# Kernel optimization log

Hardware: AMD Instinct MI355X
Metric: run time of the kernel (lower is better)

## Reference

```python
import jax, jax.numpy as jnp
import numpy as np

B, N, F, FP, H = 4, 2048, 64, 32, 4
BN_EPS = 1e-3  # tf.layers.batch_normalization default


def setup_inputs() -> dict:
    key = jax.random.key(0)
    ks = jax.random.split(key, 8)
    x = jax.random.normal(ks[0], (B, N, F), dtype=jnp.float32)
    adj = jax.random.uniform(ks[1], (B, N, N), dtype=jnp.float32)
    attn_mask = jnp.zeros((B, N, N), dtype=jnp.float32)
    # per-head parameters stacked on leading head axis
    W = jax.random.normal(ks[2], (H, F, FP), dtype=jnp.float32) * 0.1
    a_self = jax.random.normal(ks[3], (H, FP), dtype=jnp.float32) * 0.1
    a_neigh = jax.random.normal(ks[4], (H, FP), dtype=jnp.float32) * 0.1
    bias = jnp.zeros((H, FP), dtype=jnp.float32)
    # batch-norm (inference) params over concat dim H*FP
    gamma = jnp.ones((H * FP,), dtype=jnp.float32)
    beta = jnp.zeros((H * FP,), dtype=jnp.float32)
    mov_mean = jnp.zeros((H * FP,), dtype=jnp.float32)
    mov_var = jnp.ones((H * FP,), dtype=jnp.float32)
    return dict(x=x, adj=adj, attn_mask=attn_mask, W=W, a_self=a_self,
                a_neigh=a_neigh, bias=bias, gamma=gamma, beta=beta,
                mov_mean=mov_mean, mov_var=mov_var)


def reference(x, adj, attn_mask, W, a_self, a_neigh, bias, gamma, beta,
              mov_mean, mov_var):
    # features per head: [B, H, N, FP]
    feats = jnp.einsum('bnf,hfd->bhnd', x, W)
    s = jnp.einsum('bhnd,hd->bhn', feats, a_self)    # attn_for_self
    t = jnp.einsum('bhnd,hd->bhn', feats, a_neigh)   # attn_for_neighs
    dense = s[..., :, None] + t[..., None, :]        # [B, H, N, N]
    dense = jnp.where(dense > 0, dense, 0.2 * dense)  # LeakyReLU(0.2)
    dense = dense + attn_mask[:, None]
    alpha = jax.nn.softmax(dense, axis=-1)
    alpha = alpha * adj[:, None]                     # include_ew=True
    # eval mode: dropout is identity
    node_feats = jnp.einsum('bhnm,bhmd->bhnd', alpha, feats) + bias[None, :, None, :]
    # attention stats losses
    nonz = (alpha != 0).sum(axis=-1)                 # [B, H, N]
    deg = (adj != 0).sum(axis=-1)                    # [B, N]
    uloss = jnp.sum(jnp.mean((nonz - deg[:, None, :]).astype(jnp.float32), axis=-1))
    eloss = jnp.sum(jnp.mean(jnp.sum(jnp.abs(alpha), axis=-1), axis=-1))
    # concat heads -> [B, N, H*FP]
    out = jnp.transpose(node_feats, (0, 2, 1, 3)).reshape(B, N, H * FP)
    # batch norm, inference mode
    out = (out - mov_mean) * jax.lax.rsqrt(mov_var + BN_EPS) * gamma + beta
    return jax.nn.relu(out), uloss, eloss
```

## Files before the change

kernel.cpp:

```cpp
#include <hip/hip_runtime.h>


#define B_ 4
#define N_ 2048
#define F_ 64
#define FP_ 32
#define H_ 4
#define C_ 128
#define IT_ 16
#define ITILES_ (N_ / IT_)
#define JCA_ 2
#define JSPANA_ (N_ / JCA_)
#define JST_ 128
#define APAD_ 132

typedef __attribute__((ext_vector_type(8))) short short8v;
typedef __attribute__((ext_vector_type(4))) float f32x4;

__device__ __forceinline__ unsigned short f2bf(float f) {
    unsigned u = __float_as_uint(f);
    u += 0x7fffu + ((u >> 16) & 1u);
    return (unsigned short)(u >> 16);
}

__global__ __launch_bounds__(256) void prep_kernel(
    const float* __restrict__ x, const float* __restrict__ W,
    const float* __restrict__ a_self, const float* __restrict__ a_neigh,
    unsigned short* __restrict__ featsT, float* __restrict__ sbuf,
    float* __restrict__ tbuf)
{
    int blk = blockIdx.x;
    int b = blk >> 5, nt = blk & 31;
    int n0 = nt << 6;
    int t = threadIdx.x, h = t >> 6, lane = t & 63;
    int quad = lane >> 4, col = lane & 15;

    short8v bw[2][2];
    const float* Wh = W + (size_t)h * F_ * FP_;
#pragma unroll
    for (int kc = 0; kc < 2; ++kc)
#pragma unroll
        for (int dt = 0; dt < 2; ++dt)
#pragma unroll
            for (int e = 0; e < 8; ++e) {
                int f = kc * 32 + quad * 8 + e;
                bw[kc][dt][e] = (short)f2bf(Wh[f * FP_ + dt * 16 + col]);
            }
    float as0 = a_self[h * FP_ + col],  as1 = a_self[h * FP_ + 16 + col];
    float an0 = a_neigh[h * FP_ + col], an1 = a_neigh[h * FP_ + 16 + col];
    size_t hrow = ((size_t)b * H_ + h) * N_;
    size_t ftb  = ((size_t)b * H_ + h) * FP_;

    for (int ms = 0; ms < 4; ++ms) {
        int row = n0 + ms * 16 + col;
        const float* xr = x + ((size_t)b * N_ + row) * F_;
        f32x4 acc0 = {0.f, 0.f, 0.f, 0.f}, acc1 = {0.f, 0.f, 0.f, 0.f};
#pragma unroll
        for (int kc = 0; kc < 2; ++kc) {
            float4 x0 = *(const float4*)(xr + kc * 32 + quad * 8);
            float4 x1 = *(const float4*)(xr + kc * 32 + quad * 8 + 4);
            short8v av;
            av[0] = (short)f2bf(x0.x); av[1] = (short)f2bf(x0.y);
            av[2] = (short)f2bf(x0.z); av[3] = (short)f2bf(x0.w);
            av[4] = (short)f2bf(x1.x); av[5] = (short)f2bf(x1.y);
            av[6] = (short)f2bf(x1.z); av[7] = (short)f2bf(x1.w);
            acc0 = __builtin_amdgcn_mfma_f32_16x16x32_bf16(av, bw[kc][0], acc0, 0, 0, 0);
            acc1 = __builtin_amdgcn_mfma_f32_16x16x32_bf16(av, bw[kc][1], acc1, 0, 0, 0);
        }
        {
            ushort4 v0, v1;
            v0.x = f2bf(acc0[0]); v0.y = f2bf(acc0[1]);
            v0.z = f2bf(acc0[2]); v0.w = f2bf(acc0[3]);
            v1.x = f2bf(acc1[0]); v1.y = f2bf(acc1[1]);
            v1.z = f2bf(acc1[2]); v1.w = f2bf(acc1[3]);
            size_t nidx = (size_t)n0 + ms * 16 + quad * 4;
            *(ushort4*)(featsT + (ftb + col) * N_ + nidx)      = v0;
            *(ushort4*)(featsT + (ftb + 16 + col) * N_ + nidx) = v1;
        }
#pragma unroll
        for (int rr = 0; rr < 4; ++rr) {
            float sv = acc0[rr] * as0 + acc1[rr] * as1;
            float tv = acc0[rr] * an0 + acc1[rr] * an1;
#pragma unroll
            for (int off = 8; off; off >>= 1) {
                sv += __shfl_down(sv, off);
                tv += __shfl_down(tv, off);
            }
            if (col == 0) {
                int n = n0 + ms * 16 + quad * 4 + rr;
                sbuf[hrow + n] = sv;
                tbuf[hrow + n] = tv;
            }
        }
    }
}

__global__ __launch_bounds__(256) void attn_kernel(
    const float* __restrict__ adj, const float* __restrict__ msk,
    const unsigned short* __restrict__ featsT,
    const float* __restrict__ sbuf, const float* __restrict__ tbuf,
    float* __restrict__ part, float* __restrict__ lpart)
{
    __shared__ float lds_adj[IT_ * APAD_];
    __shared__ float lds_msk[IT_ * APAD_];

    int blk = blockIdx.x;
    int jc = blk & (JCA_ - 1);
    int it = (blk >> 1) & (ITILES_ - 1);
    int b  = blk >> 8;
    int t = threadIdx.x, h = t >> 6, lane = t & 63;
    int quad = lane >> 4, r = lane & 15;
    int i0 = it * IT_;
    int jbase = jc * JSPANA_;

    size_t hrow = ((size_t)b * H_ + h) * N_;
    float si = sbuf[hrow + i0 + r];
    const float* trow = tbuf + hrow + jbase;
    const unsigned short* ft0 = featsT + (((size_t)b * H_ + h) * FP_ + r) * N_ + jbase;
    const unsigned short* ft1 = ft0 + (size_t)16 * N_;
    const float* adjb = adj + ((size_t)b * N_ + i0) * N_ + jbase;
    const float* mskb = msk + ((size_t)b * N_ + i0) * N_ + jbase;

    int srow = t >> 4, sj = (t & 15) * 8;

    f32x4 acc0 = {0.f, 0.f, 0.f, 0.f}, acc1 = {0.f, 0.f, 0.f, 0.f};
    float l = 0.f, A = 0.f, nz = 0.f;

    for (int st = 0; st < JSPANA_ / JST_; ++st) {
        int j0 = st * JST_;
        __syncthreads();
        {
            const float* ga = adjb + (size_t)srow * N_ + j0 + sj;
            const float* gm = mskb + (size_t)srow * N_ + j0 + sj;
            *(float4*)&lds_adj[srow * APAD_ + sj]     = *(const float4*)ga;
            *(float4*)&lds_adj[srow * APAD_ + sj + 4] = *(const float4*)(ga + 4);
            *(float4*)&lds_msk[srow * APAD_ + sj]     = *(const float4*)gm;
            *(float4*)&lds_msk[srow * APAD_ + sj + 4] = *(const float4*)(gm + 4);
        }
        __syncthreads();
#pragma unroll
        for (int kc = 0; kc < JST_ / 32; ++kc) {
            int jt = kc * 32 + quad * 8;
            int jl = j0 + jt;
            float4 a0 = *(const float4*)&lds_adj[r * APAD_ + jt];
            float4 a1 = *(const float4*)&lds_adj[r * APAD_ + jt + 4];
            float4 m0 = *(const float4*)&lds_msk[r * APAD_ + jt];
            float4 m1 = *(const float4*)&lds_msk[r * APAD_ + jt + 4];
            float4 t0 = *(const float4*)(trow + jl);
            float4 t1 = *(const float4*)(trow + jl + 4);
            short8v bv0 = *(const short8v*)(ft0 + jl);
            short8v bv1 = *(const short8v*)(ft1 + jl);
            float av[8] = {a0.x, a0.y, a0.z, a0.w, a1.x, a1.y, a1.z, a1.w};
            float mv[8] = {m0.x, m0.y, m0.z, m0.w, m1.x, m1.y, m1.z, m1.w};
            float tv[8] = {t0.x, t0.y, t0.z, t0.w, t1.x, t1.y, t1.z, t1.w};
            short8v ap;
#pragma unroll
            for (int q = 0; q < 8; ++q) {
                float dv = si + tv[q];
                dv = fmaxf(dv, 0.2f * dv);
                dv += mv[q];
                float e = __expf(dv);
                float p = e * av[q];
                l += e; A += p;
                nz += (av[q] == 0.f ? 1.f : 0.f) - (p == 0.f ? 1.f : 0.f);
                ap[q] = (short)f2bf(p);
            }
            acc0 = __builtin_amdgcn_mfma_f32_16x16x32_bf16(ap, bv0, acc0, 0, 0, 0);
            acc1 = __builtin_amdgcn_mfma_f32_16x16x32_bf16(ap, bv1, acc1, 0, 0, 0);
        }
    }
    l  += __shfl_down(l, 32);  l  += __shfl_down(l, 16);
    A  += __shfl_down(A, 32);  A  += __shfl_down(A, 16);
    nz += __shfl_down(nz, 32); nz += __shfl_down(nz, 16);

    size_t pb = ((((size_t)(b * H_ + h) * ITILES_ + it) * JCA_ + jc) * 2) * 256;
    *(f32x4*)&part[pb + lane * 4]       = acc0;
    *(f32x4*)&part[pb + 256 + lane * 4] = acc1;
    if (lane < 16) {
        size_t lb = (((size_t)(b * H_ + h) * ITILES_ + it) * JCA_ + jc) * 48;
        lpart[lb + lane]      = l;
        lpart[lb + 16 + lane] = A;
        lpart[lb + 32 + lane] = nz;
    }
}

__global__ __launch_bounds__(256) void final_kernel(
    const float* __restrict__ part, const float* __restrict__ lpart,
    const float* __restrict__ bias, const float* __restrict__ gamma,
    const float* __restrict__ beta, const float* __restrict__ mmean,
    const float* __restrict__ mvar, float2* __restrict__ lossbuf,
    float* __restrict__ out)
{
    __shared__ float ldsl[H_ * 16];
    __shared__ float ldso[IT_ * 132];
    int blk = blockIdx.x;
    int b = blk >> 7, it = blk & 127;
    int t = threadIdx.x, h = t >> 6, lane = t & 63;
    int quad = lane >> 4, col = lane & 15;

    size_t pb = (((size_t)(b * H_ + h) * ITILES_ + it) * JCA_) * 512;
    f32x4 C0 = *(const f32x4*)&part[pb + lane * 4];
    f32x4 C1 = *(const f32x4*)&part[pb + 256 + lane * 4];
    C0 += *(const f32x4*)&part[pb + 512 + lane * 4];
    C1 += *(const f32x4*)&part[pb + 768 + lane * 4];

    size_t lb = (((size_t)(b * H_ + h) * ITILES_ + it) * JCA_) * 48;
    if (lane < 16) {
        float lt  = lpart[lb + lane]      + lpart[lb + 48 + lane];
        float At  = lpart[lb + 16 + lane] + lpart[lb + 64 + lane];
        float nzt = lpart[lb + 32 + lane] + lpart[lb + 80 + lane];
        ldsl[h * 16 + lane] = lt;
        float u = nzt, e = At / lt;
#pragma unroll
        for (int off = 8; off; off >>= 1) { u += __shfl_down(u, off); e += __shfl_down(e, off); }
        if (lane == 0) lossbuf[blk * H_ + h] = make_float2(u, e);
    }
    __syncthreads();
#pragma unroll
    for (int dt = 0; dt < 2; ++dt) {
        int c = h * FP_ + dt * 16 + col;
        float sc = rsqrtf(mvar[c] + 1e-3f) * gamma[c];
        float sh = beta[c] - mmean[c] * sc;
        float bi = bias[c];
        f32x4 Cv = dt ? C1 : C0;
#pragma unroll
        for (int rr = 0; rr < 4; ++rr) {
            int row = quad * 4 + rr;
            float node = Cv[rr] / ldsl[h * 16 + row] + bi;
            float o = node * sc + sh;
            ldso[row * 132 + c] = o > 0.f ? o : 0.f;
        }
    }
    __syncthreads();
#pragma unroll
    for (int ps = 0; ps < 2; ++ps) {
        int row = ps * 8 + (t >> 5);
        int c4 = (t & 31) * 4;
        *(float4*)(out + ((size_t)b * N_ + it * IT_ + row) * C_ + c4) =
            *(const float4*)&ldso[row * 132 + c4];
    }
}

__global__ __launch_bounds__(256) void loss_kernel(
    const float2* __restrict__ lossbuf, float* __restrict__ out)
{
    float u = 0.f, e = 0.f;
    for (int idx = threadIdx.x; idx < B_ * ITILES_ * H_; idx += 256) {
        float2 v = lossbuf[idx];
        u += v.x; e += v.y;
    }
    __shared__ float su[256], se[256];
    su[threadIdx.x] = u; se[threadIdx.x] = e;
    __syncthreads();
    for (int o = 128; o; o >>= 1) {
        if (threadIdx.x < o) {
            su[threadIdx.x] += su[threadIdx.x + o];
            se[threadIdx.x] += se[threadIdx.x + o];
        }
        __syncthreads();
    }
    if (threadIdx.x == 0) {
        out[(size_t)B_ * N_ * C_]     = su[0] * (1.f / N_);
        out[(size_t)B_ * N_ * C_ + 1] = se[0] * (1.f / N_);
    }
}

extern "C" void kernel_launch(void* const* d_in, const int* in_sizes, int n_in,
                              void* d_out, int out_size, void* d_ws, size_t ws_size,
                              hipStream_t stream)
{
    const float* x         = (const float*)d_in[0];
    const float* adj       = (const float*)d_in[1];
    const float* attn_mask = (const float*)d_in[2];
    const float* W         = (const float*)d_in[3];
    const float* a_self    = (const float*)d_in[4];
    const float* a_neigh   = (const float*)d_in[5];
    const float* bias      = (const float*)d_in[6];
    const float* gamma     = (const float*)d_in[7];
    const float* beta      = (const float*)d_in[8];
    const float* mmean     = (const float*)d_in[9];
    const float* mvar      = (const float*)d_in[10];
    float* out = (float*)d_out;

    float* ws = (float*)d_ws;
    unsigned short* featsT = (unsigned short*)ws;
    float* sbuf  = ws + 524288;
    float* tbuf  = sbuf + (size_t)B_ * H_ * N_;
    float* part  = tbuf + (size_t)B_ * H_ * N_;
    float* lpart = part + (size_t)B_ * H_ * ITILES_ * JCA_ * 2 * 256;
    float* lossb = lpart + (size_t)B_ * H_ * ITILES_ * JCA_ * 48;

    hipLaunchKernelGGL(prep_kernel, dim3(B_ * 32), dim3(256), 0, stream,
                       x, W, a_self, a_neigh, featsT, sbuf, tbuf);
    hipLaunchKernelGGL(attn_kernel, dim3(B_ * ITILES_ * JCA_), dim3(256), 0, stream,
                       adj, attn_mask, featsT, sbuf, tbuf, part, lpart);
    hipLaunchKernelGGL(final_kernel, dim3(B_ * ITILES_), dim3(256), 0, stream,
                       part, lpart, bias, gamma, beta, mmean, mvar,
                       (float2*)lossb, out);
    hipLaunchKernelGGL(loss_kernel, dim3(1), dim3(256), 0, stream,
                       (const float2*)lossb, out);
}
```

Measured before the change: 209.6 us.

## Load adj/mask directly from global, drop LDS staging, split j into 4 chunks

The attention kernel no longer stages adj and mask tiles through shared memory with barriers. Each lane now reads its own row segment straight from global memory, which removes the __syncthreads and LDS round trip. The j-range is also split into 4 chunks instead of 2, doubling the grid for more parallelism, and the final kernel sums the extra partials in a loop. The risk is less coalesced global access, since each lane reads 32 bytes per row for 16 different rows, plus more partial-sum traffic. The launch grid must also match the new chunk count, which presumably happens in code not shown.

Measured after the change: 242.8 us. 1.16x slower.

```diff
diff --git a/kernel.cpp b/kernel.cpp
--- a/kernel.cpp
+++ b/kernel.cpp
@@ -9,10 +9,8 @@
 #define C_ 128
 #define IT_ 16
 #define ITILES_ (N_ / IT_)
-#define JCA_ 2
+#define JCA_ 4
 #define JSPANA_ (N_ / JCA_)
-#define JST_ 128
-#define APAD_ 132
 
 typedef __attribute__((ext_vector_type(8))) short short8v;
 typedef __attribute__((ext_vector_type(4))) float f32x4;
@@ -101,13 +99,10 @@
     const float* __restrict__ sbuf, const float* __restrict__ tbuf,
     float* __restrict__ part, float* __restrict__ lpart)
 {
-    __shared__ float lds_adj[IT_ * APAD_];
-    __shared__ float lds_msk[IT_ * APAD_];
-
     int blk = blockIdx.x;
     int jc = blk & (JCA_ - 1);
-    int it = (blk >> 1) & (ITILES_ - 1);
-    int b  = blk >> 8;
+    int it = (blk >> 2) & (ITILES_ - 1);
+    int b  = blk >> 9;
     int t = threadIdx.x, h = t >> 6, lane = t & 63;
     int quad = lane >> 4, r = lane & 15;
     int i0 = it * IT_;
@@ -118,56 +113,40 @@
     const float* trow = tbuf + hrow + jbase;
     const unsigned short* ft0 = featsT + (((size_t)b * H_ + h) * FP_ + r) * N_ + jbase;
     const unsigned short* ft1 = ft0 + (size_t)16 * N_;
-    const float* adjb = adj + ((size_t)b * N_ + i0) * N_ + jbase;
-    const float* mskb = msk + ((size_t)b * N_ + i0) * N_ + jbase;
-
-    int srow = t >> 4, sj = (t & 15) * 8;
+    const float* adjb = adj + ((size_t)b * N_ + i0 + r) * N_ + jbase + quad * 8;
+    const float* mskb = msk + ((size_t)b * N_ + i0 + r) * N_ + jbase + quad * 8;
 
     f32x4 acc0 = {0.f, 0.f, 0.f, 0.f}, acc1 = {0.f, 0.f, 0.f, 0.f};
     float l = 0.f, A = 0.f, nz = 0.f;
 
-    for (int st = 0; st < JSPANA_ / JST_; ++st) {
-        int j0 = st * JST_;
-        __syncthreads();
-        {
-            const float* ga = adjb + (size_t)srow * N_ + j0 + sj;
-            const float* gm = mskb + (size_t)srow * N_ + j0 + sj;
-            *(float4*)&lds_adj[srow * APAD_ + sj]     = *(const float4*)ga;
-            *(float4*)&lds_adj[srow * APAD_ + sj + 4] = *(const float4*)(ga + 4);
-            *(float4*)&lds_msk[srow * APAD_ + sj]     = *(const float4*)gm;
-            *(float4*)&lds_msk[srow * APAD_ + sj + 4] = *(const float4*)(gm + 4);
-        }
-        __syncthreads();
-#pragma unroll
-        for (int kc = 0; kc < JST_ / 32; ++kc) {
-            int jt = kc * 32 + quad * 8;
-            int jl = j0 + jt;
-            float4 a0 = *(const float4*)&lds_adj[r * APAD_ + jt];
-            float4 a1 = *(const float4*)&lds_adj[r * APAD_ + jt + 4];
-            float4 m0 = *(const float4*)&lds_msk[r * APAD_ + jt];
-            float4 m1 = *(const float4*)&lds_msk[r * APAD_ + jt + 4];
-            float4 t0 = *(const float4*)(trow + jl);
-            float4 t1 = *(const float4*)(trow + jl + 4);
-            short8v bv0 = *(const short8v*)(ft0 + jl);
-            short8v bv1 = *(const short8v*)(ft1 + jl);
-            float av[8] = {a0.x, a0.y, a0.z, a0.w, a1.x, a1.y, a1.z, a1.w};
-            float mv[8] = {m0.x, m0.y, m0.z, m0.w, m1.x, m1.y, m1.z, m1.w};
-            float tv[8] = {t0.x, t0.y, t0.z, t0.w, t1.x, t1.y, t1.z, t1.w};
-            short8v ap;
-#pragma unroll
-            for (int q = 0; q < 8; ++q) {
-                float dv = si + tv[q];
-                dv = fmaxf(dv, 0.2f * dv);
-                dv += mv[q];
-                float e = __expf(dv);
-                float p = e * av[q];
-                l += e; A += p;
-                nz += (av[q] == 0.f ? 1.f : 0.f) - (p == 0.f ? 1.f : 0.f);
-                ap[q] = (short)f2bf(p);
-            }
-            acc0 = __builtin_amdgcn_mfma_f32_16x16x32_bf16(ap, bv0, acc0, 0, 0, 0);
-            acc1 = __builtin_amdgcn_mfma_f32_16x16x32_bf16(ap, bv1, acc1, 0, 0, 0);
-        }
+#pragma unroll 2
+    for (int kc = 0; kc < JSPANA_ / 32; ++kc) {
+        int jl = kc * 32 + quad * 8;
+        float4 a0 = *(const float4*)(adjb + kc * 32);
+        float4 a1 = *(const float4*)(adjb + kc * 32 + 4);
+        float4 m0 = *(const float4*)(mskb + kc * 32);
+        float4 m1 = *(const float4*)(mskb + kc * 32 + 4);
+        float4 t0 = *(const float4*)(trow + jl);
+        float4 t1 = *(const float4*)(trow + jl + 4);
+        short8v bv0 = *(const short8v*)(ft0 + jl);
+        short8v bv1 = *(const short8v*)(ft1 + jl);
+        float av[8] = {a0.x, a0.y, a0.z, a0.w, a1.x, a1.y, a1.z, a1.w};
+        float mv[8] = {m0.x, m0.y, m0.z, m0.w, m1.x, m1.y, m1.z, m1.w};
+        float tv[8] = {t0.x, t0.y, t0.z, t0.w, t1.x, t1.y, t1.z, t1.w};
+        short8v ap;
+#pragma unroll
+        for (int q = 0; q < 8; ++q) {
+            float dv = si + tv[q];
+            dv = fmaxf(dv, 0.2f * dv);
+            dv += mv[q];
+            float e = __expf(dv);
+            float p = e * av[q];
+            l += e; A += p;
+            nz += (av[q] == 0.f ? 1.f : 0.f) - (p == 0.f ? 1.f : 0.f);
+            ap[q] = (short)f2bf(p);
+        }
+        acc0 = __builtin_amdgcn_mfma_f32_16x16x32_bf16(ap, bv0, acc0, 0, 0, 0);
+        acc1 = __builtin_amdgcn_mfma_f32_16x16x32_bf16(ap, bv1, acc1, 0, 0, 0);
     }
     l  += __shfl_down(l, 32);  l  += __shfl_down(l, 16);
     A  += __shfl_down(A, 32);  A  += __shfl_down(A, 16);
@@ -199,16 +178,22 @@
     int quad = lane >> 4, col = lane & 15;
 
     size_t pb = (((size_t)(b * H_ + h) * ITILES_ + it) * JCA_) * 512;
-    f32x4 C0 = *(const f32x4*)&part[pb + lane * 4];
-    f32x4 C1 = *(const f32x4*)&part[pb + 256 + lane * 4];
-    C0 += *(const f32x4*)&part[pb + 512 + lane * 4];
-    C1 += *(const f32x4*)&part[pb + 768 + lane * 4];
+    f32x4 C0 = {0.f, 0.f, 0.f, 0.f}, C1 = {0.f, 0.f, 0.f, 0.f};
+#pragma unroll
+    for (int c = 0; c < JCA_; ++c) {
+        C0 += *(const f32x4*)&part[pb + c * 512 + lane * 4];
+        C1 += *(const f32x4*)&part[pb + c * 512 + 256 + lane * 4];
+    }
 
     size_t lb = (((size_t)(b * H_ + h) * ITILES_ + it) * JCA_) * 48;
     if (lane < 16) {
-        float lt  = lpart[lb + lane]      + lpart[lb + 48 + lane];
-        float At  = lpart[lb + 16 + lane] + lpart[lb + 64 + lane];
-        float nzt = lpart[lb + 32 + lane] + lpart[lb + 80 + lane];
+        float lt = 0.f, At = 0.f, nzt = 0.f;
+#pragma unroll
+        for (int c = 0; c < JCA_; ++c) {
+            lt  += lpart[lb + c * 48 + lane];
+            At  += lpart[lb + c * 48 + 16 + lane];
+            nzt += lpart[lb + c * 48 + 32 + lane];
+        }
         ldsl[h * 16 + lane] = lt;
         float u = nzt, e = At / lt;
 #pragma unroll
```
